# Kernel tuning notes

Hardware: AMD Instinct MI355X
Metric: run time of the kernel (lower is better)

## Reference

```python
import jax, jax.numpy as jnp
import numpy as np

TAU = 2.0        # spikingjelly LIFNode default
V_TH = 1.0       # default v_threshold
V_RESET = 0.0    # default v_reset (hard reset)


def setup_inputs() -> dict:
    key = jax.random.key(0)
    k1, k2, k3 = jax.random.split(key, 3)
    T, B, N, Cin, Cout = 4, 8, 1024, 512, 512
    x = jax.random.normal(k1, (T, B, N, Cin), dtype=jnp.float32)
    # nn.Linear weights are [out, in]; kaiming-uniform-ish scale
    W1 = jax.random.normal(k2, (Cout, Cin), dtype=jnp.float32) / np.sqrt(Cin)
    W2 = jax.random.normal(k3, (Cout, Cout), dtype=jnp.float32) / np.sqrt(Cout)
    return {"x": x, "W1": W1, "W2": W2}


def _spike(v):
    # forward heaviside (ATan surrogate only matters for backward)
    return (v >= V_TH).astype(v.dtype)


def _lif_multistep(h):
    # h: [T, B, N, C]; multi-step LIF with decay_input=True, hard reset to 0
    v0 = jnp.zeros(h.shape[1:], dtype=h.dtype)

    def step(v, x_t):
        v = v + (x_t - (v - V_RESET)) / TAU   # leaky integration
        s = _spike(v)                          # threshold
        v = v * (1.0 - s) + V_RESET * s        # hard reset
        return v, s

    _, spikes = jax.lax.scan(step, v0, h)
    return spikes  # [T, B, N, C]


def reference(x, W1, W2):
    h = jnp.einsum('tbni,oi->tbno', x, W1)      # Linear(in_ch, out_ch, bias=False)
    s = _lif_multistep(h)                        # LIFNode, step_mode='m'
    out = jnp.einsum('tbno,po->tbnp', s, W2)    # Linear(out_ch, out_ch, bias=False)
    return out.astype(jnp.float32)
```

## Files before the change

kernel.cpp:

```cpp
#include <hip/hip_runtime.h>


typedef _Float16 half8  __attribute__((ext_vector_type(8)));
typedef _Float16 half4v __attribute__((ext_vector_type(4)));
typedef float    f32x4  __attribute__((ext_vector_type(4)));
typedef float    f32x16 __attribute__((ext_vector_type(16)));
typedef unsigned short ushort8 __attribute__((ext_vector_type(8)));

constexpr int TT   = 4;
constexpr int BB   = 8;
constexpr int NN   = 1024;
constexpr int CC   = 512;
constexpr int MROW = BB * NN;
constexpr int MTOT = TT * MROW;
constexpr int BNC  = MROW * CC;
constexpr int LDK  = 40;
constexpr int LTA  = 260;

__global__ __launch_bounds__(256)
void transpose_w(const float* __restrict__ W, float* __restrict__ Wt) {
    __shared__ float T[64][65];
    const int tid = threadIdx.x;
    const int bo  = blockIdx.x * 64;
    const int bk  = blockIdx.y * 64;
#pragma unroll
    for (int j = 0; j < 16; ++j) {
        int id = tid + 256 * j;
        int r = id >> 6, c = id & 63;
        T[r][c] = W[(size_t)(bo + r) * CC + bk + c];
    }
    __syncthreads();
#pragma unroll
    for (int j = 0; j < 16; ++j) {
        int id = tid + 256 * j;
        int r = id >> 6, c = id & 63;
        Wt[(size_t)(bk + r) * CC + bo + c] = T[c][r];
    }
}

__global__ __launch_bounds__(512, 4)
void gemm1_smem(const float* __restrict__ X, const float* __restrict__ Wt,
                float* __restrict__ H) {
#pragma clang fp contract(off)
    __shared__ float At[2][32][LTA];

    const int tid  = threadIdx.x;
    const int lane = tid & 63;
    const int wid  = __builtin_amdgcn_readfirstlane(tid >> 6);
    const int RM   = blockIdx.x * 256;
    const int CN   = blockIdx.y * 128 + wid * 16;
    const float* wcol = Wt + CN;

    const int srow = tid >> 1;
    const int sk16 = (tid & 1) * 16;

    float acc[4][16] = {};
    f32x4 rx[4];

#pragma unroll
    for (int q = 0; q < 4; ++q)
        rx[q] = *(const f32x4*)&X[(size_t)(RM + srow) * CC + sk16 + q * 4];
#pragma unroll
    for (int q = 0; q < 4; ++q)
#pragma unroll
        for (int e = 0; e < 4; ++e)
            At[0][sk16 + q * 4 + e][srow] = rx[q][e];
    __syncthreads();

    for (int kt = 0; kt < 16; ++kt) {
        const int cur = kt & 1;
        if (kt < 15) {
            int kk = (kt + 1) * 32;
#pragma unroll
            for (int q = 0; q < 4; ++q)
                rx[q] = *(const f32x4*)&X[(size_t)(RM + srow) * CC + kk + sk16 + q * 4];
        }
#pragma unroll 4
        for (int k = 0; k < 32; ++k) {
            f32x4 a = *(const f32x4*)&At[cur][k][lane * 4];
            f32x16 b = *(const f32x16*)&wcol[(size_t)(kt * 32 + k) * CC];
#pragma unroll
            for (int i = 0; i < 4; ++i)
#pragma unroll
                for (int j = 0; j < 16; ++j)
                    acc[i][j] = __builtin_fmaf(a[i], b[j], acc[i][j]);
        }
        if (kt < 15) {
#pragma unroll
            for (int q = 0; q < 4; ++q)
#pragma unroll
                for (int e = 0; e < 4; ++e)
                    At[cur ^ 1][sk16 + q * 4 + e][srow] = rx[q][e];
            __syncthreads();
        }
    }

#pragma unroll
    for (int i = 0; i < 4; ++i) {
        size_t base = (size_t)(RM + lane * 4 + i) * CC + CN;
#pragma unroll
        for (int q = 0; q < 4; ++q) {
            f32x4 o = {acc[i][q * 4], acc[i][q * 4 + 1],
                       acc[i][q * 4 + 2], acc[i][q * 4 + 3]};
            *(f32x4*)&H[base + q * 4] = o;
        }
    }
}

__global__ __launch_bounds__(256)
void lif_np(const float* __restrict__ H, unsigned char* __restrict__ S8) {
#pragma clang fp contract(off)
    int g = blockIdx.x * 256 + threadIdx.x;
    float v[4] = {0.f, 0.f, 0.f, 0.f};
#pragma unroll
    for (int t = 0; t < TT; ++t) {
        f32x4 h = *(const f32x4*)&H[(size_t)t * BNC + (size_t)g * 4];
        unsigned int pack = 0;
#pragma unroll
        for (int e = 0; e < 4; ++e) {
            float d  = h[e] - v[e];
            float d2 = d * 0.5f;
            v[e] = v[e] + d2;
            bool sp = v[e] >= 1.0f;
            if (sp) { pack |= 0x3Cu << (8 * e); v[e] = 0.0f; }
        }
        *(unsigned int*)&S8[(size_t)t * BNC + (size_t)g * 4] = pack;
    }
}

__global__ __launch_bounds__(256)
void gemm2_f16(const unsigned char* __restrict__ S8, const float* __restrict__ W,
               float* __restrict__ O) {
    __shared__ _Float16 As[128][LDK], Bs[128][LDK];

    const int tid  = threadIdx.x;
    const int RM   = blockIdx.x * 128;
    const int CN   = blockIdx.y * 128;
    const int lane = tid & 63;
    const int wv   = tid >> 6;
    const int wr   = (wv >> 1) * 64;
    const int wc   = (wv & 1) * 64;
    const int r15  = lane & 15;
    const int kg   = lane >> 4;

    f32x4 acc[4][4] = {};

    for (int k0 = 0; k0 < CC; k0 += 32) {
        __syncthreads();
#pragma unroll
        for (int j = 0; j < 2; ++j) {
            int id  = tid + 256 * j;
            int row = id >> 2;
            int c8  = (id & 3) * 8;
            unsigned long long v =
                *(const unsigned long long*)&S8[(size_t)(RM + row) * CC + k0 + c8];
            ushort8 u;
#pragma unroll
            for (int e = 0; e < 8; ++e)
                u[e] = (unsigned short)(((v >> (8 * e)) & 0xFFull) << 8);
            *(ushort8*)&As[row][c8] = u;
        }
#pragma unroll
        for (int j = 0; j < 4; ++j) {
            int id  = tid + 256 * j;
            int row = id >> 3;
            int c4  = (id & 7) * 4;
            f32x4 v = *(const f32x4*)&W[(size_t)(CN + row) * CC + k0 + c4];
            half4v hv;
#pragma unroll
            for (int e = 0; e < 4; ++e) hv[e] = (_Float16)v[e];
            *(half4v*)&Bs[row][c4] = hv;
        }
        __syncthreads();

        half8 a[4], b[4];
#pragma unroll
        for (int i = 0; i < 4; ++i) {
            a[i] = *(const half8*)&As[wr + i * 16 + r15][kg * 8];
            b[i] = *(const half8*)&Bs[wc + i * 16 + r15][kg * 8];
        }
#pragma unroll
        for (int i = 0; i < 4; ++i)
#pragma unroll
            for (int j = 0; j < 4; ++j)
                acc[i][j] = __builtin_amdgcn_mfma_f32_16x16x32_f16(a[i], b[j], acc[i][j], 0, 0, 0);
    }

#pragma unroll
    for (int i = 0; i < 4; ++i)
#pragma unroll
        for (int j = 0; j < 4; ++j)
#pragma unroll
            for (int r = 0; r < 4; ++r) {
                int gm = RM + wr + i * 16 + kg * 4 + r;
                int gn = CN + wc + j * 16 + r15;
                O[(size_t)gm * CC + gn] = acc[i][j][r];
            }
}

extern "C" void kernel_launch(void* const* d_in, const int* in_sizes, int n_in,
                              void* d_out, int out_size, void* d_ws, size_t ws_size,
                              hipStream_t stream) {
    const float* x  = (const float*)d_in[0];
    const float* W1 = (const float*)d_in[1];
    const float* W2 = (const float*)d_in[2];
    float* out = (float*)d_out;

    float*         h  = out;
    unsigned char* s8 = (unsigned char*)d_ws;
    float*         wt = (float*)((char*)d_ws + (size_t)BNC);

    dim3 gt(CC / 64, CC / 64);
    transpose_w<<<gt, 256, 0, stream>>>(W1, wt);

    dim3 g1(MTOT / 256, CC / 128);
    gemm1_smem<<<g1, 512, 0, stream>>>(x, wt, h);

    lif_np<<<BNC / 4 / 256, 256, 0, stream>>>(h, s8);

    dim3 g2(MTOT / 128, CC / 128);
    gemm2_f16<<<g2, 256, 0, stream>>>(s8, W2, out);
}
```

Baseline: 239.7 us.

## Halve gemm1 per-wave column tile and software-prefetch W rows

Shrinks gemm1's per-wave output tile from 4x16 to 4x8 columns and the block's column span from 128 to 64, doubling the grid along N and reducing accumulator registers. It adds a one-step register prefetch of the next W row (two f32x4 loads) to hide global load latency, and adds a barrier before overwriting the double-buffered shared tile. The trade-off is twice as many reloads of the X tile into shared memory and lower arithmetic intensity per loaded A value, plus a launch-bounds change from 4 to 2 blocks per CU.

```diff
diff --git a/kernel.cpp b/kernel.cpp
--- a/kernel.cpp
+++ b/kernel.cpp
@@ -4,7 +4,6 @@
 typedef _Float16 half8  __attribute__((ext_vector_type(8)));
 typedef _Float16 half4v __attribute__((ext_vector_type(4)));
 typedef float    f32x4  __attribute__((ext_vector_type(4)));
-typedef float    f32x16 __attribute__((ext_vector_type(16)));
 typedef unsigned short ushort8 __attribute__((ext_vector_type(8)));
 
 constexpr int TT   = 4;
@@ -38,24 +37,25 @@
     }
 }
 
-__global__ __launch_bounds__(512, 4)
-void gemm1_smem(const float* __restrict__ X, const float* __restrict__ Wt,
-                float* __restrict__ H) {
+__global__ __launch_bounds__(512, 2)
+void gemm1_v15(const float* __restrict__ X, const float* __restrict__ Wt,
+               float* __restrict__ H) {
 #pragma clang fp contract(off)
     __shared__ float At[2][32][LTA];
 
     const int tid  = threadIdx.x;
     const int lane = tid & 63;
-    const int wid  = __builtin_amdgcn_readfirstlane(tid >> 6);
+    const int wid  = tid >> 6;
     const int RM   = blockIdx.x * 256;
-    const int CN   = blockIdx.y * 128 + wid * 16;
+    const int CN   = blockIdx.y * 64 + wid * 8;
     const float* wcol = Wt + CN;
 
     const int srow = tid >> 1;
     const int sk16 = (tid & 1) * 16;
 
-    float acc[4][16] = {};
+    float acc[4][8] = {};
     f32x4 rx[4];
+    f32x4 bc0, bc1, bn0, bn1;
 
 #pragma unroll
     for (int q = 0; q < 4; ++q)
@@ -65,6 +65,8 @@
 #pragma unroll
         for (int e = 0; e < 4; ++e)
             At[0][sk16 + q * 4 + e][srow] = rx[q][e];
+    bc0 = *(const f32x4*)&wcol[0];
+    bc1 = *(const f32x4*)&wcol[4];
     __syncthreads();
 
     for (int kt = 0; kt < 16; ++kt) {
@@ -75,17 +77,24 @@
             for (int q = 0; q < 4; ++q)
                 rx[q] = *(const f32x4*)&X[(size_t)(RM + srow) * CC + kk + sk16 + q * 4];
         }
-#pragma unroll 4
+#pragma unroll 8
         for (int k = 0; k < 32; ++k) {
+            const int gk = kt * 32 + k;
+            bn0 = *(const f32x4*)&wcol[(size_t)(gk + 1) * CC];
+            bn1 = *(const f32x4*)&wcol[(size_t)(gk + 1) * CC + 4];
             f32x4 a = *(const f32x4*)&At[cur][k][lane * 4];
-            f32x16 b = *(const f32x16*)&wcol[(size_t)(kt * 32 + k) * CC];
 #pragma unroll
             for (int i = 0; i < 4; ++i)
 #pragma unroll
-                for (int j = 0; j < 16; ++j)
-                    acc[i][j] = __builtin_fmaf(a[i], b[j], acc[i][j]);
+                for (int e = 0; e < 4; ++e) {
+                    acc[i][e]     = __builtin_fmaf(a[i], bc0[e], acc[i][e]);
+                    acc[i][4 + e] = __builtin_fmaf(a[i], bc1[e], acc[i][4 + e]);
+                }
+            bc0 = bn0;
+            bc1 = bn1;
         }
         if (kt < 15) {
+            __syncthreads();
 #pragma unroll
             for (int q = 0; q < 4; ++q)
 #pragma unroll
@@ -98,12 +107,10 @@
 #pragma unroll
     for (int i = 0; i < 4; ++i) {
         size_t base = (size_t)(RM + lane * 4 + i) * CC + CN;
-#pragma unroll
-        for (int q = 0; q < 4; ++q) {
-            f32x4 o = {acc[i][q * 4], acc[i][q * 4 + 1],
-                       acc[i][q * 4 + 2], acc[i][q * 4 + 3]};
-            *(f32x4*)&H[base + q * 4] = o;
-        }
+        f32x4 o0 = {acc[i][0], acc[i][1], acc[i][2], acc[i][3]};
+        f32x4 o1 = {acc[i][4], acc[i][5], acc[i][6], acc[i][7]};
+        *(f32x4*)&H[base]     = o0;
+        *(f32x4*)&H[base + 4] = o1;
     }
 }
 
@@ -213,8 +220,8 @@
     dim3 gt(CC / 64, CC / 64);
     transpose_w<<<gt, 256, 0, stream>>>(W1, wt);
 
-    dim3 g1(MTOT / 256, CC / 128);
-    gemm1_smem<<<g1, 512, 0, stream>>>(x, wt, h);
+    dim3 g1(MTOT / 256, CC / 64);
+    gemm1_v15<<<g1, 512, 0, stream>>>(x, wt, h);
 
     lif_np<<<BNC / 4 / 256, 256, 0, stream>>>(h, s8);
 
```

New measurement: 349.1 us. 45.7% more time.
